# Optimization experiments

Measured on AMD Instinct MI355X. Metric: run time of the kernel, lower is better.

## Reference

```python
import jax, jax.numpy as jnp
import numpy as np
import math

NUM_HEADS = 8
LN_EPS = 1e-5
SINK_EPS = 1.0  # entropic eps in SinkhornDistance (eps=1)


def _layer_norm(x, g, b):
    m = jnp.mean(x, axis=-1, keepdims=True)
    v = jnp.var(x, axis=-1, keepdims=True)
    return (x - m) * jax.lax.rsqrt(v + LN_EPS) * g + b


def setup_inputs() -> dict:
    key = jax.random.key(0)
    ks = jax.random.split(key, 8)
    B, n, dQ, dV = 8, 1024, 512, 512
    s = 1.0 / math.sqrt(dV)
    return {
        "Q": jax.random.normal(ks[0], (B, n, dQ), jnp.float32),
        "K": jax.random.normal(ks[1], (B, n, dQ), jnp.float32),
        "Wq": jax.random.normal(ks[2], (dV, dQ), jnp.float32) * s,
        "bq": jax.random.normal(ks[3], (dV,), jnp.float32) * 0.01,
        "Wo": jax.random.normal(ks[4], (dV, dV), jnp.float32) * s,
        "bo": jax.random.normal(ks[5], (dV,), jnp.float32) * 0.01,
        "g0": jnp.ones((dV,), jnp.float32),
        "b0": jnp.zeros((dV,), jnp.float32),
        "g1": jnp.ones((dV,), jnp.float32),
        "b1": jnp.zeros((dV,), jnp.float32),
    }


def reference(Q, K, Wq, bq, Wo, bo, g0, b0, g1, b1):
    # K is accepted by the original forward but unused (K_ = V_ = Q_).
    B, n, _ = Q.shape
    dim_V = Wq.shape[0]
    H = NUM_HEADS
    d = dim_V // H

    Qp = Q @ Wq.T + bq                                   # [B, n, dim_V]
    # torch.cat(Q.split(d, 2), 0): head-major stacking -> [H*B, n, d]
    Q_ = Qp.reshape(B, n, H, d).transpose(2, 0, 1, 3).reshape(H * B, n, d)

    sqrtV = math.sqrt(math.sqrt(dim_V))
    X = Q_ / sqrtV
    # cost = dotmat(X, X) = -X X^T  (overall scaled by 1/sqrt(dim_V))
    C = -jnp.einsum('bnd,bmd->bnm', X, X)                # [HB, n, n]

    # log-domain Sinkhorn, eps=1, max_iter=1, mu = nu = 1/n
    log_mu = jnp.log(1.0 / n + 1e-8).astype(Q.dtype)
    M0 = -C / SINK_EPS
    u = SINK_EPS * (log_mu - jax.scipy.special.logsumexp(M0, axis=-1))         # [HB, n]
    v = SINK_EPS * (log_mu - jax.scipy.special.logsumexp(
        (-C + u[:, :, None]) / SINK_EPS, axis=1))                               # [HB, n]
    pi = jnp.exp((-C + u[:, :, None] + v[:, None, :]) / SINK_EPS)               # [HB, n, n]

    A = pi * n
    O_ = Q_ + jnp.einsum('bnm,bmd->bnd', A, Q_)          # [HB, n, d]
    # inverse head stacking -> [B, n, dim_V]
    O = O_.reshape(H, B, n, d).transpose(1, 2, 0, 3).reshape(B, n, dim_V)

    O = _layer_norm(O, g0, b0)
    O = O + jax.nn.relu(O @ Wo.T + bo)
    O = _layer_norm(O, g1, b1)
    return O
```

## Files before the change

### kernel.cpp

```cpp
#include <hip/hip_runtime.h>
#include <hip/hip_bf16.h>

typedef __bf16 bf16;
typedef __bf16 bf16x4 __attribute__((ext_vector_type(4)));
typedef __bf16 bf16x8 __attribute__((ext_vector_type(8)));
typedef float  f32x4  __attribute__((ext_vector_type(4)));
typedef float  f32x16 __attribute__((ext_vector_type(16)));
typedef unsigned int uint32x2 __attribute__((ext_vector_type(2)));

#define DEVI static __device__ __forceinline__

constexpr float SCALE2  = 0.063758716f;
constexpr float L2MU    = -9.9999852f;
constexpr int   LDT     = 72;

DEVI f32x4 mfma16(bf16x8 a, bf16x8 b, f32x4 c) {
    return __builtin_amdgcn_mfma_f32_16x16x32_bf16(a, b, c, 0, 0, 0);
}
DEVI f32x16 mfma32(bf16x8 a, bf16x8 b, f32x16 c) {
    return __builtin_amdgcn_mfma_f32_32x32x16_bf16(a, b, c, 0, 0, 0);
}
DEVI unsigned cvtpk(float lo, float hi) {
    unsigned r;
    asm("v_cvt_pk_bf16_f32 %0, %1, %2" : "=v"(r) : "v"(lo), "v"(hi));
    return r;
}

DEVI bf16x8 cvt8(const float* __restrict__ p) {
    const float4 f0 = *(const float4*)p;
    const float4 f1 = *(const float4*)(p + 4);
    bf16x8 h;
    h[0] = (bf16)f0.x; h[1] = (bf16)f0.y; h[2] = (bf16)f0.z; h[3] = (bf16)f0.w;
    h[4] = (bf16)f1.x; h[5] = (bf16)f1.y; h[6] = (bf16)f1.z; h[7] = (bf16)f1.w;
    return h;
}

template<int EPI>
__global__ __launch_bounds__(256)
void gemm_kernel(const void* __restrict__ Ap, const float* __restrict__ Bm,
                 const float* __restrict__ bias, const bf16* __restrict__ X0,
                 bf16* __restrict__ outQh, bf16* __restrict__ outQhT,
                 float* __restrict__ outT)
{
    __shared__ bf16 sA[64 * LDT];
    __shared__ bf16 sB[64 * LDT];
    const int tid = threadIdx.x;
    const int lin = blockIdx.y * 8 + blockIdx.x;
    const int wk  = ((lin & 7) << 7) | (lin >> 3);
    const int rowBase = (wk >> 3) * 64;
    const int colBase = (wk & 7) * 64;
    const int w = tid >> 6, lane = tid & 63, quad = lane >> 4, l16 = lane & 15;
    const int wr = (w >> 1) * 32, wc = (w & 1) * 32;

    f32x4 acc[2][2];
    #pragma unroll
    for (int i = 0; i < 2; ++i)
        #pragma unroll
        for (int j = 0; j < 2; ++j)
            #pragma unroll
            for (int e = 0; e < 4; ++e) acc[i][j][e] = 0.f;

    for (int kt = 0; kt < 512; kt += 64) {
        if (kt) __syncthreads();
        #pragma unroll
        for (int it = 0; it < 2; ++it) {
            int idx = it * 256 + tid;
            int r = idx >> 3, kb = idx & 7;
            if (EPI == 0) {
                *(bf16x8*)(&sA[r * LDT + kb * 8]) =
                    cvt8((const float*)Ap + (size_t)(rowBase + r) * 512 + kt + kb * 8);
            } else {
                *(uint4*)(&sA[r * LDT + kb * 8]) =
                    *(const uint4*)((const bf16*)Ap + (size_t)(rowBase + r) * 512 + kt + kb * 8);
            }
            *(bf16x8*)(&sB[r * LDT + kb * 8]) =
                cvt8(Bm + (size_t)(colBase + r) * 512 + kt + kb * 8);
        }
        __syncthreads();
        #pragma unroll
        for (int kk = 0; kk < 2; ++kk) {
            bf16x8 a[2], b[2];
            #pragma unroll
            for (int i = 0; i < 2; ++i)
                a[i] = *(const bf16x8*)(&sA[(wr + i * 16 + l16) * LDT + kk * 32 + quad * 8]);
            #pragma unroll
            for (int j = 0; j < 2; ++j)
                b[j] = *(const bf16x8*)(&sB[(wc + j * 16 + l16) * LDT + kk * 32 + quad * 8]);
            #pragma unroll
            for (int i = 0; i < 2; ++i)
                #pragma unroll
                for (int j = 0; j < 2; ++j)
                    acc[i][j] = mfma16(a[i], b[j], acc[i][j]);
        }
    }

    #pragma unroll
    for (int i = 0; i < 2; ++i) {
        #pragma unroll
        for (int j = 0; j < 2; ++j) {
            const int col = colBase + wc + j * 16 + l16;
            const float bv = bias[col];
            if (EPI == 0) {
                const int hh = col >> 6, jj = col & 63;
                const int rowA = rowBase + wr + i * 16 + quad * 4;
                const int bb = rowA >> 10, iib = rowA & 1023;
                const int bhh = (hh << 3) + bb;
                bf16x4 pk;
                #pragma unroll
                for (int rg = 0; rg < 4; ++rg) {
                    const float z = acc[i][j][rg] + bv;
                    pk[rg] = (bf16)z;
                    outQh[((size_t)(bhh * 1024 + iib + rg) << 6) + jj] = (bf16)z;
                }
                if (outQhT)
                    *(bf16x4*)(&outQhT[(((size_t)bhh * 64 + jj) << 10) + iib]) = pk;
            } else {
                #pragma unroll
                for (int rg = 0; rg < 4; ++rg) {
                    const int row = rowBase + wr + i * 16 + quad * 4 + rg;
                    const float z = acc[i][j][rg] + bv;
                    const float x0 = (float)X0[(size_t)row * 512 + col];
                    outT[(size_t)row * 512 + col] = x0 + fmaxf(z, 0.f);
                }
            }
        }
    }
}

template<int ADD_U>
__global__ __launch_bounds__(256, 4)
void sink_lse_kernel(const bf16* __restrict__ Qh, const float* __restrict__ uin,
                     float* __restrict__ out)
{
    __shared__ bf16 sQm[2][64 * LDT];
    __shared__ float su[1024];
    const int tid = threadIdx.x;
    const int lin = blockIdx.y * 16 + blockIdx.x;
    const int wk  = ((lin & 7) << 7) | (lin >> 3);
    const int bh = wk >> 4;
    const int rowTile = (wk & 15) * 64;
    const bf16* Qb = Qh + ((size_t)bh << 16);

    if (ADD_U)
        *(float4*)(&su[tid * 4]) = *(const float4*)(uin + (bh << 10) + tid * 4);

    const int r0 = tid >> 3, kb0 = tid & 7;
    #pragma unroll
    for (int it = 0; it < 2; ++it)
        *(uint4*)(&sQm[0][(it * 32 + r0) * LDT + kb0 * 8]) =
            *(const uint4*)(Qb + ((it * 32 + r0) << 6) + kb0 * 8);

    const int w = tid >> 6, lane = tid & 63, quad = lane >> 4, l16 = lane & 15;
    bf16x8 afr[2];
    #pragma unroll
    for (int kk = 0; kk < 2; ++kk)
        afr[kk] = *(const bf16x8*)(Qb + ((rowTile + w * 16 + l16) << 6) + kk * 32 + quad * 8);
    __syncthreads();

    float rsum[4] = {0.f, 0.f, 0.f, 0.f};

    for (int mt = 0; mt < 16; ++mt) {
        const int cur = mt & 1;
        uint4 pf[2];
        if (mt < 15) {
            #pragma unroll
            for (int it = 0; it < 2; ++it)
                pf[it] = *(const uint4*)(Qb + (((mt + 1) * 64 + it * 32 + r0) << 6) + kb0 * 8);
        }

        f32x4 acc[4];
        #pragma unroll
        for (int ct = 0; ct < 4; ++ct)
            #pragma unroll
            for (int e = 0; e < 4; ++e) acc[ct][e] = 0.f;

        #pragma unroll
        for (int kk = 0; kk < 2; ++kk) {
            bf16x8 bfr[4];
            #pragma unroll
            for (int ct = 0; ct < 4; ++ct)
                bfr[ct] = *(const bf16x8*)(&sQm[cur][(ct * 16 + l16) * LDT + kk * 32 + quad * 8]);
            #pragma unroll
            for (int ct = 0; ct < 4; ++ct)
                acc[ct] = mfma16(afr[kk], bfr[ct], acc[ct]);
        }
        #pragma unroll
        for (int ct = 0; ct < 4; ++ct) {
            const float uadd = ADD_U ? su[mt * 64 + ct * 16 + l16] : 0.f;
            #pragma unroll
            for (int rg = 0; rg < 4; ++rg)
                rsum[rg] += __builtin_amdgcn_exp2f(fmaf(acc[ct][rg], SCALE2, uadd));
        }

        if (mt < 15) {
            #pragma unroll
            for (int it = 0; it < 2; ++it)
                *(uint4*)(&sQm[cur ^ 1][(it * 32 + r0) * LDT + kb0 * 8]) = pf[it];
        }
        __syncthreads();
    }
    #pragma unroll
    for (int off = 1; off < 16; off <<= 1)
        #pragma unroll
        for (int rg = 0; rg < 4; ++rg)
            rsum[rg] += __shfl_xor(rsum[rg], off);

    if (l16 == 0) {
        #pragma unroll
        for (int rg = 0; rg < 4; ++rg)
            out[(bh << 10) + rowTile + w * 16 + quad * 4 + rg] =
                L2MU - __builtin_amdgcn_logf(rsum[rg]);
    }
}

template<int USE_T>
__global__ __launch_bounds__(256, 2)
void sink_av_kernel(const bf16* __restrict__ Qh, const bf16* __restrict__ QhT,
                    const float* __restrict__ u, const float* __restrict__ v,
                    float* __restrict__ O)
{
    __shared__ bf16 sQi[128 * LDT];
    __shared__ bf16 sQm[2][64 * LDT];
    __shared__ bf16 sQmT[2][64 * LDT];
    __shared__ float sv[1024];
    const int tid = threadIdx.x;
    const int lin = blockIdx.y * 8 + blockIdx.x;
    const int wk  = ((lin & 7) << 6) | (lin >> 3);
    const int bh = wk >> 3;
    const int rowTile = (wk & 7) * 128;
    const bf16* Qb = Qh + ((size_t)bh << 16);
    const bf16* QbT = QhT + ((size_t)bh << 16);
    const int w = tid >> 6, lane = tid & 63, hi = lane >> 5, l31 = lane & 31;
    const int r0 = tid >> 3, kb0 = tid & 7;

    #pragma unroll
    for (int it = 0; it < 4; ++it) {
        int idx = it * 256 + tid;
        int r = idx >> 3, kb = idx & 7;
        *(uint4*)(&sQi[r * LDT + kb * 8]) =
            *(const uint4*)(Qb + ((rowTile + r) << 6) + kb * 8);
    }
    *(float4*)(&sv[tid * 4]) = *(const float4*)(v + (bh << 10) + tid * 4);
    const float u2p = u[(bh << 10) + rowTile + w * 32 + l31] + 10.f;

    #pragma unroll
    for (int it = 0; it < 2; ++it) {
        const int r = it * 32 + r0;
        uint4 val = *(const uint4*)(Qb + (r << 6) + kb0 * 8);
        *(uint4*)(&sQm[0][r * LDT + kb0 * 8]) = val;
        if (USE_T) {
            *(uint4*)(&sQmT[0][r * LDT + kb0 * 8]) =
                *(const uint4*)(QbT + (r << 10) + kb0 * 8);
        } else {
            union { uint4 q; bf16 e[8]; } cv; cv.q = val;
            #pragma unroll
            for (int j = 0; j < 8; ++j)
                sQmT[0][(kb0 * 8 + j) * LDT + r] = cv.e[j];
        }
    }
    __syncthreads();

    f32x16 accO[2];
    #pragma unroll
    for (int dt = 0; dt < 2; ++dt)
        #pragma unroll
        for (int e = 0; e < 16; ++e) accO[dt][e] = 0.f;

    for (int mt = 0; mt < 16; ++mt) {
        const int cur = mt & 1;
        uint4 pfm[2], pft[2];
        if (mt < 15) {
            #pragma unroll
            for (int it = 0; it < 2; ++it) {
                const int r = it * 32 + r0;
                pfm[it] = *(const uint4*)(Qb + (((mt + 1) * 64 + r) << 6) + kb0 * 8);
                if (USE_T)
                    pft[it] = *(const uint4*)(QbT + (r << 10) + (mt + 1) * 64 + kb0 * 8);
            }
        }

        f32x16 accT[2];
        #pragma unroll
        for (int t = 0; t < 2; ++t)
            #pragma unroll
            for (int e = 0; e < 16; ++e) accT[t][e] = 0.f;
        #pragma unroll
        for (int ks = 0; ks < 4; ++ks) {
            const bf16x8 bq = *(const bf16x8*)(&sQi[(w * 32 + l31) * LDT + ks * 16 + hi * 8]);
            #pragma unroll
            for (int t = 0; t < 2; ++t) {
                const bf16x8 am = *(const bf16x8*)(&sQm[cur][(t * 32 + l31) * LDT + ks * 16 + hi * 8]);
                accT[t] = mfma32(am, bq, accT[t]);
            }
        }

        bf16x8 pa[4];
        #pragma unroll
        for (int t = 0; t < 2; ++t) {
            f32x4 vf[4];
            #pragma unroll
            for (int g = 0; g < 4; ++g)
                vf[g] = *(const f32x4*)(&sv[mt * 64 + t * 32 + g * 8 + hi * 4]);
            float p[16];
            #pragma unroll
            for (int r = 0; r < 16; ++r)
                p[r] = __builtin_amdgcn_exp2f(
                         fmaf(accT[t][r], SCALE2, u2p + vf[r >> 2][r & 3]));
            #pragma unroll
            for (int kk = 0; kk < 2; ++kk) {
                const int rb = kk * 8;
                unsigned X0 = cvtpk(p[rb + 0], p[rb + 1]);
                unsigned Y0 = cvtpk(p[rb + 4], p[rb + 5]);
                unsigned X1 = cvtpk(p[rb + 2], p[rb + 3]);
                unsigned Y1 = cvtpk(p[rb + 6], p[rb + 7]);
                uint32x2 s0 = __builtin_amdgcn_permlane32_swap(X0, Y0, false, false);
                uint32x2 s1 = __builtin_amdgcn_permlane32_swap(X1, Y1, false, false);
                union { unsigned wd[4]; bf16x8 v8; } u4;
                u4.wd[0] = s0[0]; u4.wd[1] = s1[0]; u4.wd[2] = s0[1]; u4.wd[3] = s1[1];
                pa[t * 2 + kk] = u4.v8;
            }
        }

        #pragma unroll
        for (int ks = 0; ks < 4; ++ks)
            #pragma unroll
            for (int dt = 0; dt < 2; ++dt) {
                const bf16x8 bt = *(const bf16x8*)(&sQmT[cur][(dt * 32 + l31) * LDT + ks * 16 + hi * 8]);
                accO[dt] = mfma32(pa[ks], bt, accO[dt]);
            }

        if (mt < 15) {
            #pragma unroll
            for (int it = 0; it < 2; ++it) {
                const int r = it * 32 + r0;
                *(uint4*)(&sQm[cur ^ 1][r * LDT + kb0 * 8]) = pfm[it];
                if (USE_T) {
                    *(uint4*)(&sQmT[cur ^ 1][r * LDT + kb0 * 8]) = pft[it];
                } else {
                    union { uint4 q; bf16 e[8]; } cv; cv.q = pfm[it];
                    #pragma unroll
                    for (int j = 0; j < 8; ++j)
                        sQmT[cur ^ 1][(kb0 * 8 + j) * LDT + r] = cv.e[j];
                }
            }
        }
        __syncthreads();
    }

    const int hh = bh >> 3, bb = bh & 7;
    #pragma unroll
    for (int dt = 0; dt < 2; ++dt) {
        const int dcol = dt * 32 + l31;
        #pragma unroll
        for (int r = 0; r < 16; ++r) {
            const int irow = w * 32 + (r & 3) + 8 * (r >> 2) + 4 * hi;
            const float o = (float)sQi[irow * LDT + dcol] + accO[dt][r];
            O[((size_t)(bb * 1024 + rowTile + irow) << 9) + (hh << 6) + dcol] = o;
        }
    }
}

template<typename OutT>
__global__ __launch_bounds__(256)
void ln_kernel(const float* __restrict__ X, const float* __restrict__ g,
               const float* __restrict__ bb, OutT* __restrict__ out)
{
    const int row = blockIdx.x;
    const float* x = X + (size_t)row * 512;
    const float2 v2 = ((const float2*)x)[threadIdx.x];
    float s  = v2.x + v2.y;
    float ss = v2.x * v2.x + v2.y * v2.y;
    #pragma unroll
    for (int off = 32; off; off >>= 1) {
        s  += __shfl_down(s, off);
        ss += __shfl_down(ss, off);
    }
    __shared__ float red[8];
    const int w = threadIdx.x >> 6, lane = threadIdx.x & 63;
    if (lane == 0) { red[w] = s; red[4 + w] = ss; }
    __syncthreads();
    s  = red[0] + red[1] + red[2] + red[3];
    ss = red[4] + red[5] + red[6] + red[7];
    const float mean = s * (1.f / 512.f);
    const float var  = ss * (1.f / 512.f) - mean * mean;
    const float rstd = rsqrtf(var + 1e-5f);
    const int c = threadIdx.x * 2;
    const float y0 = (v2.x - mean) * rstd * g[c]     + bb[c];
    const float y1 = (v2.y - mean) * rstd * g[c + 1] + bb[c + 1];
    out[(size_t)row * 512 + c]     = (OutT)y0;
    out[(size_t)row * 512 + c + 1] = (OutT)y1;
}

extern "C" void kernel_launch(void* const* d_in, const int* in_sizes, int n_in,
                              void* d_out, int out_size, void* d_ws, size_t ws_size,
                              hipStream_t stream)
{
    const float* Q  = (const float*)d_in[0];
    const float* Wq = (const float*)d_in[2];
    const float* bq = (const float*)d_in[3];
    const float* Wo = (const float*)d_in[4];
    const float* bo = (const float*)d_in[5];
    const float* g0 = (const float*)d_in[6];
    const float* b0 = (const float*)d_in[7];
    const float* g1 = (const float*)d_in[8];
    const float* b1 = (const float*)d_in[9];

    char* ws = (char*)d_ws;
    const bool useT = ws_size >= (size_t)34078720;

    bf16 *Qh, *QhT, *X0;
    float *u, *v, *Obuf;
    if (useT) {
        Qh   = (bf16*)ws;
        QhT  = (bf16*)(ws + 8388608);
        X0   = (bf16*)(ws + 8388608);
        u    = (float*)(ws + 16777216);
        v    = (float*)(ws + 17039360);
        Obuf = (float*)(ws + 17301504);
    } else {
        Qh   = (bf16*)ws;
        QhT  = nullptr;
        X0   = (bf16*)ws;
        u    = (float*)(ws + 8388608);
        v    = (float*)(ws + 8650752);
        Obuf = (float*)(ws + 8912896);
    }

    gemm_kernel<0><<<dim3(8, 128), 256, 0, stream>>>(Q, Wq, bq, nullptr, Qh, QhT, nullptr);
    sink_lse_kernel<0><<<dim3(16, 64), 256, 0, stream>>>(Qh, nullptr, u);
    sink_lse_kernel<1><<<dim3(16, 64), 256, 0, stream>>>(Qh, u, v);
    if (useT)
        sink_av_kernel<1><<<dim3(8, 64), 256, 0, stream>>>(Qh, QhT, u, v, Obuf);
    else
        sink_av_kernel<0><<<dim3(8, 64), 256, 0, stream>>>(Qh, Qh, u, v, Obuf);
    ln_kernel<bf16><<<8192, 256, 0, stream>>>(Obuf, g0, b0, X0);
    gemm_kernel<1><<<dim3(8, 128), 256, 0, stream>>>(X0, Wo, bo, X0, nullptr, nullptr, Obuf);
    ln_kernel<float><<<8192, 256, 0, stream>>>(Obuf, g1, b1, (float*)d_out);
}
```

Measured before the change: 203.8 us.

## Double-buffer GEMM tiles, pre-convert weights to bf16, vectorize layer norm

Adds a small kernel that converts Wq and Wo to bf16 in workspace, so the GEMMs load bf16 B tiles directly instead of converting fp32 on every tile load. The GEMM main loop now uses two shared-memory buffers with register prefetch of the next k-tile. This overlaps global loads with MFMA work and needs one barrier per iteration instead of two. LayerNorm is rewritten to handle one row per wave with float4 loads and xor shuffles, removing the shared-memory reduction and block barrier. The cost is two extra launches and workspace aliasing that depends on buffer lifetimes.

```diff
diff --git a/kernel.cpp b/kernel.cpp
--- a/kernel.cpp
+++ b/kernel.cpp
@@ -35,15 +35,22 @@
     return h;
 }
 
+__global__ __launch_bounds__(256)
+void cvtw_kernel(const float* __restrict__ W, bf16* __restrict__ Wb)
+{
+    const int i = (blockIdx.x * 256 + threadIdx.x) * 8;
+    *(bf16x8*)(&Wb[i]) = cvt8(W + i);
+}
+
 template<int EPI>
 __global__ __launch_bounds__(256)
-void gemm_kernel(const void* __restrict__ Ap, const float* __restrict__ Bm,
+void gemm_kernel(const void* __restrict__ Ap, const bf16* __restrict__ Bb,
                  const float* __restrict__ bias, const bf16* __restrict__ X0,
                  bf16* __restrict__ outQh, bf16* __restrict__ outQhT,
                  float* __restrict__ outT)
 {
-    __shared__ bf16 sA[64 * LDT];
-    __shared__ bf16 sB[64 * LDT];
+    __shared__ bf16 sA[2][64 * LDT];
+    __shared__ bf16 sB[2][64 * LDT];
     const int tid = threadIdx.x;
     const int lin = blockIdx.y * 8 + blockIdx.x;
     const int wk  = ((lin & 7) << 7) | (lin >> 3);
@@ -51,6 +58,7 @@
     const int colBase = (wk & 7) * 64;
     const int w = tid >> 6, lane = tid & 63, quad = lane >> 4, l16 = lane & 15;
     const int wr = (w >> 1) * 32, wc = (w & 1) * 32;
+    const int r0 = tid >> 3, kb0 = tid & 7;
 
     f32x4 acc[2][2];
     #pragma unroll
@@ -60,38 +68,74 @@
             #pragma unroll
             for (int e = 0; e < 4; ++e) acc[i][j][e] = 0.f;
 
-    for (int kt = 0; kt < 512; kt += 64) {
-        if (kt) __syncthreads();
-        #pragma unroll
-        for (int it = 0; it < 2; ++it) {
-            int idx = it * 256 + tid;
-            int r = idx >> 3, kb = idx & 7;
-            if (EPI == 0) {
-                *(bf16x8*)(&sA[r * LDT + kb * 8]) =
-                    cvt8((const float*)Ap + (size_t)(rowBase + r) * 512 + kt + kb * 8);
-            } else {
-                *(uint4*)(&sA[r * LDT + kb * 8]) =
-                    *(const uint4*)((const bf16*)Ap + (size_t)(rowBase + r) * 512 + kt + kb * 8);
-            }
-            *(bf16x8*)(&sB[r * LDT + kb * 8]) =
-                cvt8(Bm + (size_t)(colBase + r) * 512 + kt + kb * 8);
-        }
-        __syncthreads();
+    #pragma unroll
+    for (int it = 0; it < 2; ++it) {
+        const int r = it * 32 + r0;
+        if (EPI == 0)
+            *(bf16x8*)(&sA[0][r * LDT + kb0 * 8]) =
+                cvt8((const float*)Ap + (size_t)(rowBase + r) * 512 + kb0 * 8);
+        else
+            *(uint4*)(&sA[0][r * LDT + kb0 * 8]) =
+                *(const uint4*)((const bf16*)Ap + (size_t)(rowBase + r) * 512 + kb0 * 8);
+        *(uint4*)(&sB[0][r * LDT + kb0 * 8]) =
+            *(const uint4*)(Bb + (size_t)(colBase + r) * 512 + kb0 * 8);
+    }
+    __syncthreads();
+
+    for (int kt8 = 0; kt8 < 8; ++kt8) {
+        const int cur = kt8 & 1;
+        float4 pfa[2][2];
+        uint4  pfa16[2], pfb[2];
+        if (kt8 < 7) {
+            const int kn = (kt8 + 1) * 64;
+            #pragma unroll
+            for (int it = 0; it < 2; ++it) {
+                const int r = it * 32 + r0;
+                if (EPI == 0) {
+                    const float* ap = (const float*)Ap + (size_t)(rowBase + r) * 512 + kn + kb0 * 8;
+                    pfa[it][0] = *(const float4*)ap;
+                    pfa[it][1] = *(const float4*)(ap + 4);
+                } else {
+                    pfa16[it] = *(const uint4*)((const bf16*)Ap + (size_t)(rowBase + r) * 512 + kn + kb0 * 8);
+                }
+                pfb[it] = *(const uint4*)(Bb + (size_t)(colBase + r) * 512 + kn + kb0 * 8);
+            }
+        }
+
         #pragma unroll
         for (int kk = 0; kk < 2; ++kk) {
             bf16x8 a[2], b[2];
             #pragma unroll
             for (int i = 0; i < 2; ++i)
-                a[i] = *(const bf16x8*)(&sA[(wr + i * 16 + l16) * LDT + kk * 32 + quad * 8]);
+                a[i] = *(const bf16x8*)(&sA[cur][(wr + i * 16 + l16) * LDT + kk * 32 + quad * 8]);
             #pragma unroll
             for (int j = 0; j < 2; ++j)
-                b[j] = *(const bf16x8*)(&sB[(wc + j * 16 + l16) * LDT + kk * 32 + quad * 8]);
+                b[j] = *(const bf16x8*)(&sB[cur][(wc + j * 16 + l16) * LDT + kk * 32 + quad * 8]);
             #pragma unroll
             for (int i = 0; i < 2; ++i)
                 #pragma unroll
                 for (int j = 0; j < 2; ++j)
                     acc[i][j] = mfma16(a[i], b[j], acc[i][j]);
         }
+
+        if (kt8 < 7) {
+            #pragma unroll
+            for (int it = 0; it < 2; ++it) {
+                const int r = it * 32 + r0;
+                if (EPI == 0) {
+                    bf16x8 h;
+                    h[0] = (bf16)pfa[it][0].x; h[1] = (bf16)pfa[it][0].y;
+                    h[2] = (bf16)pfa[it][0].z; h[3] = (bf16)pfa[it][0].w;
+                    h[4] = (bf16)pfa[it][1].x; h[5] = (bf16)pfa[it][1].y;
+                    h[6] = (bf16)pfa[it][1].z; h[7] = (bf16)pfa[it][1].w;
+                    *(bf16x8*)(&sA[cur ^ 1][r * LDT + kb0 * 8]) = h;
+                } else {
+                    *(uint4*)(&sA[cur ^ 1][r * LDT + kb0 * 8]) = pfa16[it];
+                }
+                *(uint4*)(&sB[cur ^ 1][r * LDT + kb0 * 8]) = pfb[it];
+            }
+        }
+        __syncthreads();
     }
 
     #pragma unroll
@@ -365,30 +409,44 @@
 void ln_kernel(const float* __restrict__ X, const float* __restrict__ g,
                const float* __restrict__ bb, OutT* __restrict__ out)
 {
-    const int row = blockIdx.x;
-    const float* x = X + (size_t)row * 512;
-    const float2 v2 = ((const float2*)x)[threadIdx.x];
-    float s  = v2.x + v2.y;
-    float ss = v2.x * v2.x + v2.y * v2.y;
+    const int row = blockIdx.x * 4 + (threadIdx.x >> 6);
+    const int lane = threadIdx.x & 63;
+    const float* x = X + (size_t)row * 512 + lane * 8;
+    const float4 a0 = *(const float4*)x;
+    const float4 a1 = *(const float4*)(x + 4);
+    float s  = a0.x + a0.y + a0.z + a0.w + a1.x + a1.y + a1.z + a1.w;
+    float ss = a0.x*a0.x + a0.y*a0.y + a0.z*a0.z + a0.w*a0.w
+             + a1.x*a1.x + a1.y*a1.y + a1.z*a1.z + a1.w*a1.w;
     #pragma unroll
     for (int off = 32; off; off >>= 1) {
-        s  += __shfl_down(s, off);
-        ss += __shfl_down(ss, off);
-    }
-    __shared__ float red[8];
-    const int w = threadIdx.x >> 6, lane = threadIdx.x & 63;
-    if (lane == 0) { red[w] = s; red[4 + w] = ss; }
-    __syncthreads();
-    s  = red[0] + red[1] + red[2] + red[3];
-    ss = red[4] + red[5] + red[6] + red[7];
+        s  += __shfl_xor(s, off);
+        ss += __shfl_xor(ss, off);
+    }
     const float mean = s * (1.f / 512.f);
-    const float var  = ss * (1.f / 512.f) - mean * mean;
-    const float rstd = rsqrtf(var + 1e-5f);
-    const int c = threadIdx.x * 2;
-    const float y0 = (v2.x - mean) * rstd * g[c]     + bb[c];
-    const float y1 = (v2.y - mean) * rstd * g[c + 1] + bb[c + 1];
-    out[(size_t)row * 512 + c]     = (OutT)y0;
-    out[(size_t)row * 512 + c + 1] = (OutT)y1;
+    const float rstd = rsqrtf(ss * (1.f / 512.f) - mean * mean + 1e-5f);
+    const int c = lane * 8;
+    const float4 g0 = *(const float4*)(g + c),  g1 = *(const float4*)(g + c + 4);
+    const float4 b0 = *(const float4*)(bb + c), b1 = *(const float4*)(bb + c + 4);
+    float y[8];
+    y[0] = (a0.x - mean) * rstd * g0.x + b0.x;
+    y[1] = (a0.y - mean) * rstd * g0.y + b0.y;
+    y[2] = (a0.z - mean) * rstd * g0.z + b0.z;
+    y[3] = (a0.w - mean) * rstd * g0.w + b0.w;
+    y[4] = (a1.x - mean) * rstd * g1.x + b1.x;
+    y[5] = (a1.y - mean) * rstd * g1.y + b1.y;
+    y[6] = (a1.z - mean) * rstd * g1.z + b1.z;
+    y[7] = (a1.w - mean) * rstd * g1.w + b1.w;
+    if constexpr (sizeof(OutT) == 2) {
+        bf16x8 h;
+        #pragma unroll
+        for (int j = 0; j < 8; ++j) h[j] = (bf16)y[j];
+        *(bf16x8*)((bf16*)out + (size_t)row * 512 + c) = h;
+    } else {
+        float4 o0 = {y[0], y[1], y[2], y[3]};
+        float4 o1 = {y[4], y[5], y[6], y[7]};
+        *(float4*)((float*)out + (size_t)row * 512 + c)     = o0;
+        *(float4*)((float*)out + (size_t)row * 512 + c + 4) = o1;
+    }
 }
 
 extern "C" void kernel_launch(void* const* d_in, const int* in_sizes, int n_in,
@@ -408,7 +466,7 @@
     char* ws = (char*)d_ws;
     const bool useT = ws_size >= (size_t)34078720;
 
-    bf16 *Qh, *QhT, *X0;
+    bf16 *Qh, *QhT, *X0, *Wqb, *Wob;
     float *u, *v, *Obuf;
     if (useT) {
         Qh   = (bf16*)ws;
@@ -417,6 +475,8 @@
         u    = (float*)(ws + 16777216);
         v    = (float*)(ws + 17039360);
         Obuf = (float*)(ws + 17301504);
+        Wqb  = (bf16*)(ws + 16777216);
+        Wob  = (bf16*)ws;
     } else {
         Qh   = (bf16*)ws;
         QhT  = nullptr;
@@ -424,16 +484,20 @@
         u    = (float*)(ws + 8388608);
         v    = (float*)(ws + 8650752);
         Obuf = (float*)(ws + 8912896);
-    }
-
-    gemm_kernel<0><<<dim3(8, 128), 256, 0, stream>>>(Q, Wq, bq, nullptr, Qh, QhT, nullptr);
+        Wqb  = (bf16*)(ws + 8388608);
+        Wob  = (bf16*)(ws + 8388608);
+    }
+
+    cvtw_kernel<<<128, 256, 0, stream>>>(Wq, Wqb);
+    gemm_kernel<0><<<dim3(8, 128), 256, 0, stream>>>(Q, Wqb, bq, nullptr, Qh, QhT, nullptr);
     sink_lse_kernel<0><<<dim3(16, 64), 256, 0, stream>>>(Qh, nullptr, u);
     sink_lse_kernel<1><<<dim3(16, 64), 256, 0, stream>>>(Qh, u, v);
     if (useT)
         sink_av_kernel<1><<<dim3(8, 64), 256, 0, stream>>>(Qh, QhT, u, v, Obuf);
     else
         sink_av_kernel<0><<<dim3(8, 64), 256, 0, stream>>>(Qh, Qh, u, v, Obuf);
-    ln_kernel<bf16><<<8192, 256, 0, stream>>>(Obuf, g0, b0, X0);
-    gemm_kernel<1><<<dim3(8, 128), 256, 0, stream>>>(X0, Wo, bo, X0, nullptr, nullptr, Obuf);
-    ln_kernel<float><<<8192, 256, 0, stream>>>(Obuf, g1, b1, (float*)d_out);
-}
+    cvtw_kernel<<<128, 256, 0, stream>>>(Wo, Wob);
+    ln_kernel<bf16><<<2048, 256, 0, stream>>>(Obuf, g0, b0, X0);
+    gemm_kernel<1><<<dim3(8, 128), 256, 0, stream>>>(X0, Wob, bo, X0, nullptr, nullptr, Obuf);
+    ln_kernel<float><<<2048, 256, 0, stream>>>(Obuf, g1, b1, (float*)d_out);
+}
```

Result: faster. 199.6 us (-2.0%).
